# Performance work log

Measured on AMD Instinct MI355X. Metric: run time of the kernel, lower is better.

## Reference

```python
import jax, jax.numpy as jnp
import numpy as np

N = 1_000_000      # occupied voxels
GRID = 256         # voxel grid extent per axis
K = 27             # 3^3 kernel offsets
CIN, COUT = 2, 16


def _build_nbr_map(coords: np.ndarray) -> np.ndarray:
    """Kernel-offset neighbor map like MinkowskiEngine's kernel map.
    coords: [N,3] unique int voxel coords. Returns [N,K] int32, -1 = no neighbor.
    """
    key = (coords[:, 0] * GRID + coords[:, 1]) * GRID + coords[:, 2]
    order = np.argsort(key)
    skey = key[order]
    offsets = np.array([[dx, dy, dz]
                        for dx in (-1, 0, 1)
                        for dy in (-1, 0, 1)
                        for dz in (-1, 0, 1)], dtype=np.int64)
    nbr = np.full((coords.shape[0], K), -1, dtype=np.int32)
    for k in range(K):
        nc = coords + offsets[k]
        valid = np.all((nc >= 0) & (nc < GRID), axis=1)
        nkey = (nc[:, 0] * GRID + nc[:, 1]) * GRID + nc[:, 2]
        pos = np.clip(np.searchsorted(skey, nkey), 0, coords.shape[0] - 1)
        hit = valid & (skey[pos] == nkey)
        nbr[:, k] = np.where(hit, order[pos].astype(np.int32), -1)
    return nbr


def setup_inputs() -> dict:
    rng = np.random.default_rng(0)
    lin = rng.choice(GRID ** 3, size=N, replace=False)  # unique voxel ids
    coords = np.stack([lin // (GRID * GRID), (lin // GRID) % GRID, lin % GRID],
                      axis=1).astype(np.int64)
    nbr = _build_nbr_map(coords)
    key = jax.random.key(0)
    k1, k2 = jax.random.split(key)
    features = jax.random.normal(k1, (N, CIN), dtype=jnp.float32)
    # MinkowskiConvolution kernel: one [Cin,Cout] matrix per kernel offset, no bias
    kernel = jax.random.normal(k2, (K, CIN, COUT), dtype=jnp.float32) * 0.1
    return {"features": features, "kernel": kernel, "nbr_idx": jnp.asarray(nbr)}


def reference(features, kernel, nbr_idx):
    # gather-GEMM-scatter sparse conv: out[n] = sum_k W_k^T x[nbr(n,k)]
    mask = (nbr_idx >= 0)
    safe = jnp.maximum(nbr_idx, 0)
    gathered = features[safe]                              # [N,K,Cin]
    gathered = gathered * mask[..., None].astype(features.dtype)
    return jnp.einsum('nkc,kcd->nd', gathered, kernel)     # [N,Cout]
```

## Files before the change

### kernel.cpp

```cpp
#include <hip/hip_runtime.h>

#define K_OFF 27
#define CIN   2
#define COUT  16
#define BLK   256
#define WPB   4
#define IPW   (64 * K_OFF)
#define NB    8

typedef __attribute__((address_space(3))) unsigned int lds_u32;
typedef __attribute__((address_space(1))) const unsigned int g_u32;

__global__ __launch_bounds__(BLK, 2) void spconv_kernel(
    const float* __restrict__ feats,
    const float* __restrict__ w,
    const int*   __restrict__ nbr,
    float*       __restrict__ out,
    int n_pts)
{
    __shared__ int    s_idx[WPB * IPW];
    __shared__ float4 s_w[8 * K_OFF];

    const int t    = threadIdx.x;
    const int lane = t & 63;
    const int wv   = t >> 6;
    const int tile = blockIdx.x * WPB + wv;
    const int p    = tile * 64 + lane;

    if (t < 8 * K_OFF) {
        const int k = t >> 3, q = t & 7;
        s_w[q * K_OFF + k] = reinterpret_cast<const float4*>(w)[t];
    }

    const bool full = ((tile + 1) * 64 <= n_pts);
    if (full) {
        const int* src = nbr + (size_t)tile * IPW;
        int*       dst = s_idx + wv * IPW;
        #pragma unroll
        for (int j = 0; j < 6; ++j) {
            __builtin_amdgcn_global_load_lds(
                (g_u32*)(src + j * 256 + lane * 4),
                (lds_u32*)(dst + j * 256), 16, 0, 0);
        }
        if (lane < 48) {
            __builtin_amdgcn_global_load_lds(
                (g_u32*)(src + 6 * 256 + lane * 4),
                (lds_u32*)(dst + 6 * 256), 16, 0, 0);
        }
    }
    __syncthreads();

    float acc[COUT];
    #pragma unroll
    for (int d = 0; d < COUT; ++d) acc[d] = 0.f;

    const float2* feats2 = reinterpret_cast<const float2*>(feats);
    const int* rowp = s_idx + wv * IPW + lane * K_OFF;

    unsigned bm = 0;
    if (full) {
        #pragma unroll
        for (int k = 0; k < K_OFF; ++k)
            bm |= (rowp[k] >= 0) ? (1u << k) : 0u;
    }

    int mx = __popc(bm);
    #pragma unroll
    for (int off = 32; off; off >>= 1) mx = max(mx, __shfl_xor(mx, off, 64));

    for (int j0 = 0; j0 < mx; j0 += NB) {
        int   kk[NB]; float fm[NB];
        #pragma unroll
        for (int j = 0; j < NB; ++j) {
            const bool alive = (bm != 0);
            kk[j] = alive ? (int)__builtin_ctz(bm) : 0;
            fm[j] = alive ? 1.0f : 0.0f;
            bm &= bm - 1;
        }
        int idx[NB];
        #pragma unroll
        for (int j = 0; j < NB; ++j) idx[j] = rowp[kk[j]];
        float2 f[NB];
        #pragma unroll
        for (int j = 0; j < NB; ++j)
            f[j] = feats2[(fm[j] > 0.f && idx[j] > 0) ? idx[j] : 0];
        #pragma unroll
        for (int j = 0; j < NB; ++j) {
            const float fx = f[j].x * fm[j], fy = f[j].y * fm[j];
            const int k = kk[j];
            #pragma unroll
            for (int q = 0; q < 4; ++q) {
                const float4 wa = s_w[q * K_OFF + k];
                const float4 wb = s_w[(q + 4) * K_OFF + k];
                acc[q*4+0] = fmaf(fy, wb.x, fmaf(fx, wa.x, acc[q*4+0]));
                acc[q*4+1] = fmaf(fy, wb.y, fmaf(fx, wa.y, acc[q*4+1]));
                acc[q*4+2] = fmaf(fy, wb.z, fmaf(fx, wa.z, acc[q*4+2]));
                acc[q*4+3] = fmaf(fy, wb.w, fmaf(fx, wa.w, acc[q*4+3]));
            }
        }
    }

    if (!full) {
        const bool pv = (p < n_pts);
        for (int k = 0; k < K_OFF; ++k) {
            const int idx = pv ? nbr[(size_t)p * K_OFF + k] : -1;
            const float fm2 = (idx >= 0) ? 1.0f : 0.0f;
            const float2 f = feats2[idx > 0 ? idx : 0];
            const float fx = f.x * fm2, fy = f.y * fm2;
            #pragma unroll
            for (int q = 0; q < 4; ++q) {
                const float4 wa = s_w[q * K_OFF + k];
                const float4 wb = s_w[(q + 4) * K_OFF + k];
                acc[q*4+0] = fmaf(fy, wb.x, fmaf(fx, wa.x, acc[q*4+0]));
                acc[q*4+1] = fmaf(fy, wb.y, fmaf(fx, wa.y, acc[q*4+1]));
                acc[q*4+2] = fmaf(fy, wb.z, fmaf(fx, wa.z, acc[q*4+2]));
                acc[q*4+3] = fmaf(fy, wb.w, fmaf(fx, wa.w, acc[q*4+3]));
            }
        }
    }

    if (p < n_pts) {
        float4* o = reinterpret_cast<float4*>(out + (size_t)p * COUT);
        o[0] = make_float4(acc[0],  acc[1],  acc[2],  acc[3]);
        o[1] = make_float4(acc[4],  acc[5],  acc[6],  acc[7]);
        o[2] = make_float4(acc[8],  acc[9],  acc[10], acc[11]);
        o[3] = make_float4(acc[12], acc[13], acc[14], acc[15]);
    }
}

extern "C" void kernel_launch(void* const* d_in, const int* in_sizes, int n_in,
                              void* d_out, int out_size, void* d_ws, size_t ws_size,
                              hipStream_t stream) {
    const float* feats = (const float*)d_in[0];
    const float* w     = (const float*)d_in[1];
    const int*   nbr   = (const int*)d_in[2];
    float*       out   = (float*)d_out;

    const int n_pts   = in_sizes[0] / CIN;
    const int n_tiles = (n_pts + 63) / 64;
    const int grid    = (n_tiles + WPB - 1) / WPB;

    spconv_kernel<<<grid, BLK, 0, stream>>>(feats, w, nbr, out, n_pts);
}
```

Baseline: 54.58 us.

## Pack features to bf16 pairs before gather, add nontemporal stores

Adds a pre-pass kernel that rounds each point's two fp32 features to bf16 and packs them into one 32-bit word in workspace. The main kernel then gathers 4-byte words instead of 8-byte float2, halving random-gather bytes, and unpacks with shifts. It also sets a cache-policy bit on the async neighbor-index loads and uses nontemporal stores for the output. This trades input precision (bf16 rounding of features) and an extra kernel launch plus an extra pass over the features for a smaller gather footprint.

```diff
diff --git a/kernel.cpp b/kernel.cpp
--- a/kernel.cpp
+++ b/kernel.cpp
@@ -10,9 +10,24 @@
 
 typedef __attribute__((address_space(3))) unsigned int lds_u32;
 typedef __attribute__((address_space(1))) const unsigned int g_u32;
+typedef float __attribute__((ext_vector_type(4))) f32x4;
+
+__global__ __launch_bounds__(256) void pack_feats_kernel(
+    const float2* __restrict__ feats2, unsigned* __restrict__ pkf, int n)
+{
+    const int i = blockIdx.x * 256 + threadIdx.x;
+    if (i < n) {
+        const float2 f = feats2[i];
+        unsigned bx = __float_as_uint(f.x);
+        unsigned by = __float_as_uint(f.y);
+        bx = (bx + 0x7FFFu + ((bx >> 16) & 1u)) >> 16;
+        by = (by + 0x7FFFu + ((by >> 16) & 1u)) >> 16;
+        pkf[i] = bx | (by << 16);
+    }
+}
 
 __global__ __launch_bounds__(BLK, 2) void spconv_kernel(
-    const float* __restrict__ feats,
+    const unsigned* __restrict__ pkf,
     const float* __restrict__ w,
     const int*   __restrict__ nbr,
     float*       __restrict__ out,
@@ -40,12 +55,12 @@
         for (int j = 0; j < 6; ++j) {
             __builtin_amdgcn_global_load_lds(
                 (g_u32*)(src + j * 256 + lane * 4),
-                (lds_u32*)(dst + j * 256), 16, 0, 0);
+                (lds_u32*)(dst + j * 256), 16, 0, 2 );
         }
         if (lane < 48) {
             __builtin_amdgcn_global_load_lds(
                 (g_u32*)(src + 6 * 256 + lane * 4),
-                (lds_u32*)(dst + 6 * 256), 16, 0, 0);
+                (lds_u32*)(dst + 6 * 256), 16, 0, 2);
         }
     }
     __syncthreads();
@@ -54,7 +69,6 @@
     #pragma unroll
     for (int d = 0; d < COUT; ++d) acc[d] = 0.f;
 
-    const float2* feats2 = reinterpret_cast<const float2*>(feats);
     const int* rowp = s_idx + wv * IPW + lane * K_OFF;
 
     unsigned bm = 0;
@@ -80,13 +94,14 @@
         int idx[NB];
         #pragma unroll
         for (int j = 0; j < NB; ++j) idx[j] = rowp[kk[j]];
-        float2 f[NB];
+        unsigned u[NB];
         #pragma unroll
         for (int j = 0; j < NB; ++j)
-            f[j] = feats2[(fm[j] > 0.f && idx[j] > 0) ? idx[j] : 0];
+            u[j] = pkf[(fm[j] > 0.f && idx[j] > 0) ? idx[j] : 0];
         #pragma unroll
         for (int j = 0; j < NB; ++j) {
-            const float fx = f[j].x * fm[j], fy = f[j].y * fm[j];
+            const float fx = __uint_as_float(u[j] << 16) * fm[j];
+            const float fy = __uint_as_float(u[j] & 0xFFFF0000u) * fm[j];
             const int k = kk[j];
             #pragma unroll
             for (int q = 0; q < 4; ++q) {
@@ -105,8 +120,9 @@
         for (int k = 0; k < K_OFF; ++k) {
             const int idx = pv ? nbr[(size_t)p * K_OFF + k] : -1;
             const float fm2 = (idx >= 0) ? 1.0f : 0.0f;
-            const float2 f = feats2[idx > 0 ? idx : 0];
-            const float fx = f.x * fm2, fy = f.y * fm2;
+            const unsigned uu = pkf[idx > 0 ? idx : 0];
+            const float fx = __uint_as_float(uu << 16) * fm2;
+            const float fy = __uint_as_float(uu & 0xFFFF0000u) * fm2;
             #pragma unroll
             for (int q = 0; q < 4; ++q) {
                 const float4 wa = s_w[q * K_OFF + k];
@@ -120,11 +136,11 @@
     }
 
     if (p < n_pts) {
-        float4* o = reinterpret_cast<float4*>(out + (size_t)p * COUT);
-        o[0] = make_float4(acc[0],  acc[1],  acc[2],  acc[3]);
-        o[1] = make_float4(acc[4],  acc[5],  acc[6],  acc[7]);
-        o[2] = make_float4(acc[8],  acc[9],  acc[10], acc[11]);
-        o[3] = make_float4(acc[12], acc[13], acc[14], acc[15]);
+        f32x4* o = reinterpret_cast<f32x4*>(out + (size_t)p * COUT);
+        __builtin_nontemporal_store((f32x4){acc[0],  acc[1],  acc[2],  acc[3]},  o + 0);
+        __builtin_nontemporal_store((f32x4){acc[4],  acc[5],  acc[6],  acc[7]},  o + 1);
+        __builtin_nontemporal_store((f32x4){acc[8],  acc[9],  acc[10], acc[11]}, o + 2);
+        __builtin_nontemporal_store((f32x4){acc[12], acc[13], acc[14], acc[15]}, o + 3);
     }
 }
 
@@ -135,10 +151,13 @@
     const float* w     = (const float*)d_in[1];
     const int*   nbr   = (const int*)d_in[2];
     float*       out   = (float*)d_out;
+    unsigned*    pkf   = (unsigned*)d_ws;
 
     const int n_pts   = in_sizes[0] / CIN;
     const int n_tiles = (n_pts + 63) / 64;
     const int grid    = (n_tiles + WPB - 1) / WPB;
 
-    spconv_kernel<<<grid, BLK, 0, stream>>>(feats, w, nbr, out, n_pts);
+    pack_feats_kernel<<<(n_pts + 255) / 256, 256, 0, stream>>>(
+        reinterpret_cast<const float2*>(feats), pkf, n_pts);
+    spconv_kernel<<<grid, BLK, 0, stream>>>(pkf, w, nbr, out, n_pts);
 }
```

Measured after the change: 65.26 us. +19.6%, slower.
